# Performance work log

Hardware: AMD Instinct MI355X
Metric: run time of the kernel (lower is better)

## Reference

```python
import jax, jax.numpy as jnp
import numpy as np

B, C, V, L = 32, 32, 1024, 13  # batch, channels, nodes, seq_len
SUPPORT_LEN, ORDER = 3, 2
C_IN_TOTAL = (ORDER * SUPPORT_LEN + 1) * C  # 224
C_OUT = 64


def setup_inputs() -> dict:
    key = jax.random.key(0)
    ks = jax.random.split(key, 6)
    x = jax.random.normal(ks[0], (B, C, V, L), dtype=jnp.float32)
    # row-normalized random adjacencies (dense diffusion matrices)
    def adj(k):
        a = jax.random.uniform(k, (V, V), dtype=jnp.float32)
        return a / jnp.sum(a, axis=1, keepdims=True)
    A0, A1, A2 = adj(ks[1]), adj(ks[2]), adj(ks[3])
    W = jax.random.normal(ks[4], (C_OUT, C_IN_TOTAL), dtype=jnp.float32) * (1.0 / np.sqrt(C_IN_TOTAL))
    b = jnp.zeros((C_OUT,), dtype=jnp.float32)
    return {"x": x, "A0": A0, "A1": A1, "A2": A2, "W": W, "b": b}


def nconv(x, A):
    # x: [b, c, v, l], A: [v, w] -> [b, c, w, l]
    return jnp.einsum('bcvl,vw->bcwl', x, A)


def reference(x, A0, A1, A2, W, b):
    out = [x]
    for A in (A0, A1, A2):
        x1 = nconv(x, A)
        out.append(x1)
        for _ in range(2, ORDER + 1):
            x2 = nconv(x1, A)
            out.append(x2)
            x1 = x2
    h = jnp.concatenate(out, axis=1)  # [b, (order*support_len+1)*c, v, l]
    # 1x1 conv == channel contraction; dropout is identity in eval mode
    return jnp.einsum('bcvl,oc->bovl', h, W) + b[None, :, None, None]
```

## Files before the change

### kernel.cpp

```cpp
#include <hip/hip_runtime.h>
#include <hip/hip_bf16.h>
#include <cstdint>


#define SZE 13631488ull
#define OFF_AT  190840832ull
#define OFF_WB  197132288ull
#define WS_NEED 197160960ull

typedef __attribute__((ext_vector_type(8))) short short8;
typedef __attribute__((ext_vector_type(4))) float f32x4;

__device__ __forceinline__ unsigned short f2b(float f) {
    unsigned int u = __builtin_bit_cast(unsigned int, f);
    u += 0x7FFFu + ((u >> 16) & 1u);
    return (unsigned short)(u >> 16);
}

__device__ __forceinline__ void gl2lds16(const unsigned short* g, unsigned short* l) {
    __builtin_amdgcn_global_load_lds(
        (__attribute__((address_space(1))) void*)(g),
        (__attribute__((address_space(3))) void*)(l), 16, 0, 0);
}

__global__ __launch_bounds__(256) void k_prep(const float* __restrict__ x,
                                              unsigned short* __restrict__ T,
                                              unsigned short* __restrict__ Ht) {
    __shared__ unsigned short sb[32 * 840];
    const int b = blockIdx.x >> 4, vc = blockIdx.x & 15;
    const int t = threadIdx.x;
    const float4* xb = (const float4*)x;
    for (int it = 0; it < 26; ++it) {
        int q = it * 256 + t;
        int c = q / 208, f = q - c * 208;
        float4 u = xb[(size_t)(b * 32 + c) * 3328 + vc * 208 + f];
        ushort4 pk; pk.x = f2b(u.x); pk.y = f2b(u.y); pk.z = f2b(u.z); pk.w = f2b(u.w);
        *(ushort4*)(sb + c * 840 + f * 4) = pk;
    }
    __syncthreads();
    unsigned short* Tb = T + (size_t)b * 13 * 32 * 1024 + (size_t)vc * 64;
    for (int it = 0; it < 26; ++it) {
        int q = it * 256 + t;
        int l = q >> 9, r = q & 511, c = r >> 4, sg = r & 15;
        const unsigned short* src = sb + c * 840 + l;
        ushort4 pk;
        pk.x = src[(sg * 4 + 0) * 13];
        pk.y = src[(sg * 4 + 1) * 13];
        pk.z = src[(sg * 4 + 2) * 13];
        pk.w = src[(sg * 4 + 3) * 13];
        *(ushort4*)(Tb + (size_t)(l * 32 + c) * 1024 + sg * 4) = pk;
    }
    unsigned short* Hb = Ht + ((size_t)b * 13312 + (size_t)vc * 832) * 224;
    for (int it = 0; it < 26; ++it) {
        int q = it * 256 + t;
        int v = q / 104, r = q - v * 104, l = r >> 3, cs = r & 7;
        const unsigned short* src = sb + v * 13 + l;
        ushort4 pk;
        pk.x = src[(cs * 4 + 0) * 840];
        pk.y = src[(cs * 4 + 1) * 840];
        pk.z = src[(cs * 4 + 2) * 840];
        pk.w = src[(cs * 4 + 3) * 840];
        *(ushort4*)(Hb + (size_t)(v * 13 + l) * 224 + cs * 4) = pk;
    }
}

__global__ __launch_bounds__(256) void k_prep_A(const float* __restrict__ A0,
                                                const float* __restrict__ A1,
                                                const float* __restrict__ A2,
                                                unsigned short* __restrict__ AT,
                                                unsigned short* __restrict__ Abf) {
    const float* A = blockIdx.z == 0 ? A0 : blockIdx.z == 1 ? A1 : A2;
    unsigned short* D = AT + (size_t)blockIdx.z * 1024 * 1024;
    unsigned short* D2 = Abf + (size_t)blockIdx.z * 1024 * 1024;
    __shared__ float tile[32][33];
    int v0 = blockIdx.y * 32, w0 = blockIdx.x * 32;
    int c = threadIdx.x & 31, r = threadIdx.x >> 5;
    for (int p = 0; p < 4; ++p) {
        int rr = r + p * 8;
        float val = A[(size_t)(v0 + rr) * 1024 + w0 + c];
        tile[rr][c] = val;
        D2[(size_t)(v0 + rr) * 1024 + w0 + c] = f2b(val);
    }
    __syncthreads();
    for (int p = 0; p < 4; ++p) {
        int rr = r + p * 8;
        D[(size_t)(w0 + rr) * 1024 + v0 + c] = f2b(tile[c][rr]);
    }
}

__global__ __launch_bounds__(256) void k_prep_W(const float* __restrict__ W,
                                                unsigned short* __restrict__ Wb) {
    int idx = blockIdx.x * 256 + threadIdx.x;
    Wb[idx] = f2b(W[idx]);
}

__global__ __launch_bounds__(256) void k_gemm(const unsigned short* __restrict__ Xb, long xz,
                                              const unsigned short* __restrict__ P0,
                                              const unsigned short* __restrict__ P1,
                                              unsigned short* __restrict__ Tout, long tz,
                                              unsigned short* __restrict__ Ht, int doT) {
    __shared__ union {
        struct { unsigned short xs[8192]; unsigned short ps[8192]; } s;
        unsigned short cs[128 * 132];
    } lds;
    const int z = blockIdx.z;
    const unsigned short* X = Xb + (size_t)z * (size_t)xz;
    const unsigned short* P = (z < 3) ? P0 + (size_t)z * 1048576u
                                      : P1 + (size_t)(z - 3) * 1048576u;
    const int i0 = blockIdx.x * 128;
    const int j0 = blockIdx.y * 128;
    const int t = threadIdx.x;
    const int lane = t & 63, wave = t >> 6;
    const int l16 = lane & 15, quad = lane >> 4;
    const int wi = (wave >> 1) * 64, wj = (wave & 1) * 64;

    f32x4 acc[4][4] = {};

    const int row = t >> 2, seg = t & 3;
    const unsigned short* xg0 = X + (size_t)(i0 + row) * 1024 + seg * 8;
    const unsigned short* xg1 = xg0 + (size_t)64 * 1024;
    const unsigned short* pg0 = P + (size_t)(j0 + row) * 1024 + seg * 8;
    const unsigned short* pg1 = pg0 + (size_t)64 * 1024;
    unsigned short* lx0 = lds.s.xs + t * 8;
    unsigned short* lp0 = lds.s.ps + t * 8;

    for (int kt = 0; kt < 16; ++kt) {
        const int ko = kt * 64;
        gl2lds16(xg0 + ko,      lx0);
        gl2lds16(xg1 + ko,      lx0 + 2048);
        gl2lds16(xg0 + ko + 32, lx0 + 4096);
        gl2lds16(xg1 + ko + 32, lx0 + 6144);
        gl2lds16(pg0 + ko,      lp0);
        gl2lds16(pg1 + ko,      lp0 + 2048);
        gl2lds16(pg0 + ko + 32, lp0 + 4096);
        gl2lds16(pg1 + ko + 32, lp0 + 6144);
        __syncthreads();
#pragma unroll
        for (int p = 0; p < 2; ++p) {
            short8 a[4], b[4];
#pragma unroll
            for (int mi = 0; mi < 4; ++mi)
                a[mi] = *(const short8*)(lds.s.xs + p * 4096 + (wi + mi * 16 + l16) * 32 + quad * 8);
#pragma unroll
            for (int nj = 0; nj < 4; ++nj)
                b[nj] = *(const short8*)(lds.s.ps + p * 4096 + (wj + nj * 16 + l16) * 32 + quad * 8);
#pragma unroll
            for (int mi = 0; mi < 4; ++mi)
#pragma unroll
                for (int nj = 0; nj < 4; ++nj)
                    acc[mi][nj] = __builtin_amdgcn_mfma_f32_16x16x32_bf16(a[mi], b[nj], acc[mi][nj], 0, 0, 0);
        }
        __syncthreads();
    }

    if (doT) {
#pragma unroll
        for (int mi = 0; mi < 4; ++mi)
#pragma unroll
            for (int nj = 0; nj < 4; ++nj)
#pragma unroll
                for (int r = 0; r < 4; ++r)
                    lds.cs[(wi + mi * 16 + quad * 4 + r) * 132 + (wj + nj * 16 + l16)] =
                        f2b(acc[mi][nj][r]);
        __syncthreads();
        unsigned short* O = Tout + (size_t)z * (size_t)tz;
#pragma unroll
        for (int rep = 0; rep < 8; ++rep) {
            int q = rep * 256 + t;
            int rr = q >> 4, sg = q & 15;
            *(uint4*)(O + (size_t)(i0 + rr) * 1024 + j0 + sg * 8) =
                *(const uint4*)(lds.cs + rr * 132 + sg * 8);
        }
    }
}

__global__ __launch_bounds__(512, 2) void k_gemm256(
        const unsigned short* __restrict__ Xb,
        const unsigned short* __restrict__ P0,
        const unsigned short* __restrict__ P1,
        unsigned short* __restrict__ Ht) {
    __shared__ unsigned short lds[65536];
    const int comb = blockIdx.x;
    const int z = comb >> 2;
    const int j0 = (comb & 3) * 256;
    const int i0 = blockIdx.y * 256;
    const unsigned short* P = (z < 3) ? P0 + (size_t)z * 1048576u
                                      : P1 + (size_t)(z - 3) * 1048576u;
    const int t = threadIdx.x;
    const int lane = t & 63;
    const int l16 = lane & 15, quad = lane >> 4;
    const int wave = t >> 6, wm = wave >> 2, wn = wave & 3;

    const unsigned short* pa0 = Xb + (size_t)(i0 + (t >> 2)) * 1024 + (t & 3) * 8;
    const unsigned short* pb0 = P  + (size_t)(j0 + (t >> 2)) * 1024 + (t & 3) * 8;

    const int aoff = (wm * 128 + l16) * 32 + quad * 8;
    const int boff = 16384 + (wn * 64 + l16) * 32 + quad * 8;

    auto stage = [&](int H) {
        if (H >= 64) return;
        const int kt = H >> 2, h = H & 3;
        const int ks = h >> 1;
        const unsigned short* s = ((h & 1) ? pb0 : pa0) + kt * 64 + ks * 32;
        unsigned short* d = lds + (kt & 1) * 32768 + (h & 1) * 16384 + ks * 8192 + t * 8;
        gl2lds16(s, d);
        gl2lds16(s + 131072, d + 4096);
    };

    f32x4 acc[8][4] = {};

#pragma unroll
    for (int H = 0; H < 7; ++H) stage(H);
    asm volatile("s_waitcnt vmcnt(6)" ::: "memory");
    __builtin_amdgcn_s_barrier();

#pragma unroll 1
    for (int kt = 0; kt < 16; ++kt) {
        const int base = (kt & 1) * 32768;
        const int P4 = kt * 4;
        short8 a[8], b0, b1;

#pragma unroll
        for (int mi = 0; mi < 8; ++mi)
            a[mi] = *(const short8*)(lds + base + aoff + mi * 512);
        b0 = *(const short8*)(lds + base + boff);
        b1 = *(const short8*)(lds + base + boff + 512);
        stage(P4 + 7);
        __builtin_amdgcn_sched_barrier(0);
        __builtin_amdgcn_s_barrier();
        asm volatile("s_waitcnt lgkmcnt(0)" ::: "memory");
        __builtin_amdgcn_sched_barrier(0);
        __builtin_amdgcn_s_setprio(1);
#pragma unroll
        for (int mi = 0; mi < 8; ++mi) {
            acc[mi][0] = __builtin_amdgcn_mfma_f32_16x16x32_bf16(a[mi], b0, acc[mi][0], 0, 0, 0);
            acc[mi][1] = __builtin_amdgcn_mfma_f32_16x16x32_bf16(a[mi], b1, acc[mi][1], 0, 0, 0);
        }
        __builtin_amdgcn_s_setprio(0);
        __builtin_amdgcn_sched_barrier(0);
        __builtin_amdgcn_s_barrier();

        b0 = *(const short8*)(lds + base + boff + 2 * 512);
        b1 = *(const short8*)(lds + base + boff + 3 * 512);
        stage(P4 + 8);
        __builtin_amdgcn_sched_barrier(0);
        __builtin_amdgcn_s_barrier();
        asm volatile("s_waitcnt lgkmcnt(0)" ::: "memory");
        __builtin_amdgcn_sched_barrier(0);
        __builtin_amdgcn_s_setprio(1);
#pragma unroll
        for (int mi = 0; mi < 8; ++mi) {
            acc[mi][2] = __builtin_amdgcn_mfma_f32_16x16x32_bf16(a[mi], b0, acc[mi][2], 0, 0, 0);
            acc[mi][3] = __builtin_amdgcn_mfma_f32_16x16x32_bf16(a[mi], b1, acc[mi][3], 0, 0, 0);
        }
        __builtin_amdgcn_s_setprio(0);
        __builtin_amdgcn_sched_barrier(0);
        __builtin_amdgcn_s_barrier();

#pragma unroll
        for (int mi = 0; mi < 8; ++mi)
            a[mi] = *(const short8*)(lds + base + 8192 + aoff + mi * 512);
        b0 = *(const short8*)(lds + base + 8192 + boff);
        b1 = *(const short8*)(lds + base + 8192 + boff + 512);
        stage(P4 + 9);
        __builtin_amdgcn_sched_barrier(0);
        __builtin_amdgcn_s_barrier();
        asm volatile("s_waitcnt lgkmcnt(0)" ::: "memory");
        __builtin_amdgcn_sched_barrier(0);
        __builtin_amdgcn_s_setprio(1);
#pragma unroll
        for (int mi = 0; mi < 8; ++mi) {
            acc[mi][0] = __builtin_amdgcn_mfma_f32_16x16x32_bf16(a[mi], b0, acc[mi][0], 0, 0, 0);
            acc[mi][1] = __builtin_amdgcn_mfma_f32_16x16x32_bf16(a[mi], b1, acc[mi][1], 0, 0, 0);
        }
        __builtin_amdgcn_s_setprio(0);
        __builtin_amdgcn_sched_barrier(0);
        __builtin_amdgcn_s_barrier();

        b0 = *(const short8*)(lds + base + 8192 + boff + 2 * 512);
        b1 = *(const short8*)(lds + base + 8192 + boff + 3 * 512);
        stage(P4 + 10);
        if (kt < 14)       asm volatile("s_waitcnt vmcnt(6)" ::: "memory");
        else if (kt == 14) asm volatile("s_waitcnt vmcnt(0)" ::: "memory");
        __builtin_amdgcn_sched_barrier(0);
        __builtin_amdgcn_s_barrier();
        asm volatile("s_waitcnt lgkmcnt(0)" ::: "memory");
        __builtin_amdgcn_sched_barrier(0);
        __builtin_amdgcn_s_setprio(1);
#pragma unroll
        for (int mi = 0; mi < 8; ++mi) {
            acc[mi][2] = __builtin_amdgcn_mfma_f32_16x16x32_bf16(a[mi], b0, acc[mi][2], 0, 0, 0);
            acc[mi][3] = __builtin_amdgcn_mfma_f32_16x16x32_bf16(a[mi], b1, acc[mi][3], 0, 0, 0);
        }
        __builtin_amdgcn_s_setprio(0);
        __builtin_amdgcn_sched_barrier(0);
        __builtin_amdgcn_s_barrier();
    }

    const int cc0 = (z < 3) ? 32 + 64 * z : 64 * (z - 2);
    const int wc = j0 + wn * 64 + l16;
#pragma unroll
    for (int mi = 0; mi < 8; ++mi) {
        int p = (i0 >> 5) + wm * 4 + (mi >> 1);
        int b = p / 13, l = p - b * 13;
        int cc = cc0 + (mi & 1) * 16 + quad * 4;
#pragma unroll
        for (int nj = 0; nj < 4; ++nj) {
            int w = wc + nj * 16;
            size_t m = (size_t)b * 13312 + (size_t)w * 13 + l;
            ushort4 pk;
            pk.x = f2b(acc[mi][nj][0]);
            pk.y = f2b(acc[mi][nj][1]);
            pk.z = f2b(acc[mi][nj][2]);
            pk.w = f2b(acc[mi][nj][3]);
            *(ushort4*)(Ht + m * 224 + cc) = pk;
        }
    }
}

__global__ __launch_bounds__(256) void k_fc(const unsigned short* __restrict__ Ht,
                                            const unsigned short* __restrict__ Wb,
                                            const float* __restrict__ bias,
                                            float* __restrict__ y) {
    __shared__ unsigned short sw[64 * 232];
    const int bid = blockIdx.x;
    const int b = bid >> 5, v0 = (bid & 31) * 32;
    const int t = threadIdx.x;
    const int lane = t & 63, wave = t >> 6;
    const int ms = wave >> 1, os = wave & 1;
    const int l16 = lane & 15, quad = lane >> 4;

    for (int it = 0; it < 7; ++it) {
        int q = it * 256 + t;
        int o = q / 28, sg = q % 28;
        *(uint4*)(sw + o * 232 + sg * 8) = *(const uint4*)(Wb + o * 224 + sg * 8);
    }

    const size_t mw = (size_t)b * 13312 + (size_t)v0 * 13 + ms * 208;
    const unsigned short* ag = Ht + (mw + l16) * 224 + quad * 8;
    float* yb = y + (size_t)b * 851968 + (size_t)v0 * 13 + ms * 208 + quad * 4;

    float bv[2];
#pragma unroll
    for (int nj = 0; nj < 2; ++nj) bv[nj] = bias[os * 32 + nj * 16 + l16];

    short8 c0[7], c1[7];
#pragma unroll
    for (int kk = 0; kk < 7; ++kk) {
        c0[kk] = *(const short8*)(ag + kk * 32);
        c1[kk] = *(const short8*)(ag + 3584 + kk * 32);
    }
    __syncthreads();

    auto body = [&](int mf, short8 (&cur)[7]) {
        short8 nxt[7];
        const bool pf = (mf + 2 < 13);
        if (pf) {
#pragma unroll
            for (int kk = 0; kk < 7; ++kk)
                nxt[kk] = *(const short8*)(ag + (size_t)(mf + 2) * 3584 + kk * 32);
        }
        f32x4 acc[2];
#pragma unroll
        for (int nj = 0; nj < 2; ++nj) acc[nj] = (f32x4){bv[nj], bv[nj], bv[nj], bv[nj]};
#pragma unroll
        for (int kk = 0; kk < 7; ++kk)
#pragma unroll
            for (int nj = 0; nj < 2; ++nj) {
                short8 bf = *(const short8*)(sw + (os * 32 + nj * 16 + l16) * 232 + kk * 32 + quad * 8);
                acc[nj] = __builtin_amdgcn_mfma_f32_16x16x32_bf16(cur[kk], bf, acc[nj], 0, 0, 0);
            }
#pragma unroll
        for (int nj = 0; nj < 2; ++nj)
            *(f32x4*)(yb + (size_t)(os * 32 + nj * 16 + l16) * 13312 + mf * 16) = acc[nj];
        if (pf) {
#pragma unroll
            for (int kk = 0; kk < 7; ++kk) cur[kk] = nxt[kk];
        }
    };
#pragma unroll
    for (int mf = 0; mf < 13; ++mf) {
        if (mf & 1) body(mf, c1); else body(mf, c0);
    }
}

extern "C" void kernel_launch(void* const* d_in, const int* in_sizes, int n_in,
                              void* d_out, int out_size, void* d_ws, size_t ws_size,
                              hipStream_t stream) {
    const float* x    = (const float*)d_in[0];
    const float* A0   = (const float*)d_in[1];
    const float* A1   = (const float*)d_in[2];
    const float* A2   = (const float*)d_in[3];
    const float* W    = (const float*)d_in[4];
    const float* bias = (const float*)d_in[5];

    if (ws_size < WS_NEED) return;

    unsigned short* Ht = (unsigned short*)d_ws;
    unsigned short* AT = (unsigned short*)((char*)d_ws + OFF_AT);
    unsigned short* Wb = (unsigned short*)((char*)d_ws + OFF_WB);
    unsigned short* Tarena = (unsigned short*)d_out;
    unsigned short* Abf = Tarena + SZE;
    unsigned short* AT2 = Tarena + 2 * SZE;

    k_prep<<<512, 256, 0, stream>>>(x, Tarena, Ht);
    k_prep_A<<<dim3(32, 32, 3), 256, 0, stream>>>(A0, A1, A2, AT, Abf);
    k_prep_W<<<56, 256, 0, stream>>>(W, Wb);
    k_gemm<<<dim3(8, 8, 3), 256, 0, stream>>>(AT, 1048576L, Abf, Abf,
                                              AT2, 1048576L, nullptr, 1);
    k_gemm256<<<dim3(24, 52, 1), 512, 0, stream>>>(Tarena, AT, AT2, Ht);
    k_fc<<<1024, 256, 0, stream>>>(Ht, Wb, bias, (float*)d_out);
}
```

Before: 464.9 us.

## Load B operand directly from global to registers and halve LDS in k_gemm256

The 256x256 GEMM kernel no longer stages the B (adjacency) tile in LDS. Each wave now loads its B fragments straight from global memory into registers, double-buffered across k-steps, while only the A tile is staged through LDS with an XOR swizzle to avoid bank conflicts. The fine-grained barrier, setprio and sched_barrier choreography is replaced by a simpler two-buffer loop with one __syncthreads per half-iteration. This halves LDS use and cuts LDS traffic, at the cost of uncoalesced-ish direct global loads for B and less explicit control over instruction scheduling.

```diff
diff --git a/kernel.cpp b/kernel.cpp
--- a/kernel.cpp
+++ b/kernel.cpp
@@ -179,7 +179,7 @@
         const unsigned short* __restrict__ P0,
         const unsigned short* __restrict__ P1,
         unsigned short* __restrict__ Ht) {
-    __shared__ unsigned short lds[65536];
+    __shared__ unsigned short lds[32768];
     const int comb = blockIdx.x;
     const int z = comb >> 2;
     const int j0 = (comb & 3) * 256;
@@ -191,110 +191,63 @@
     const int l16 = lane & 15, quad = lane >> 4;
     const int wave = t >> 6, wm = wave >> 2, wn = wave & 3;
 
-    const unsigned short* pa0 = Xb + (size_t)(i0 + (t >> 2)) * 1024 + (t & 3) * 8;
-    const unsigned short* pb0 = P  + (size_t)(j0 + (t >> 2)) * 1024 + (t & 3) * 8;
-
-    const int aoff = (wm * 128 + l16) * 32 + quad * 8;
-    const int boff = 16384 + (wn * 64 + l16) * 32 + quad * 8;
-
-    auto stage = [&](int H) {
-        if (H >= 64) return;
-        const int kt = H >> 2, h = H & 3;
-        const int ks = h >> 1;
-        const unsigned short* s = ((h & 1) ? pb0 : pa0) + kt * 64 + ks * 32;
-        unsigned short* d = lds + (kt & 1) * 32768 + (h & 1) * 16384 + ks * 8192 + t * 8;
-        gl2lds16(s, d);
-        gl2lds16(s + 131072, d + 4096);
+    const unsigned short* pa0 = Xb + (size_t)(i0 + (t >> 3)) * 1024
+                                   + (size_t)(((t & 7) ^ ((t >> 3) & 7)) * 8);
+    auto stage = [&](int kt, int buf) {
+        const unsigned short* s = pa0 + kt * 64;
+        unsigned short* d = lds + buf * 16384 + t * 8;
+#pragma unroll
+        for (int sw = 0; sw < 4; ++sw)
+            gl2lds16(s + sw * 65536, d + sw * 4096);
     };
 
+    const int abase = (wm * 128 + l16) * 64 + ((quad ^ (l16 & 7)) * 8);
+    const unsigned short* pbl = P + (size_t)(j0 + wn * 64 + l16) * 1024 + quad * 8;
+
     f32x4 acc[8][4] = {};
-
-#pragma unroll
-    for (int H = 0; H < 7; ++H) stage(H);
-    asm volatile("s_waitcnt vmcnt(6)" ::: "memory");
-    __builtin_amdgcn_s_barrier();
+    short8 bA[4], bB[4];
+
+    auto ldb = [&](short8* dst, int g) {
+#pragma unroll
+        for (int nj = 0; nj < 4; ++nj)
+            dst[nj] = *(const short8*)(pbl + nj * 16384 + g * 32);
+    };
+    auto ksstep = [&](const unsigned short* ab, int koff, short8* bu) {
+        short8 a[8];
+#pragma unroll
+        for (int mi = 0; mi < 8; ++mi)
+            a[mi] = *(const short8*)(ab + koff + mi * 1024);
+#pragma unroll
+        for (int mi = 0; mi < 8; ++mi)
+#pragma unroll
+            for (int nj = 0; nj < 4; ++nj)
+                acc[mi][nj] = __builtin_amdgcn_mfma_f32_16x16x32_bf16(a[mi], bu[nj], acc[mi][nj], 0, 0, 0);
+    };
+
+    stage(0, 0);
+    ldb(bA, 0);
+    __syncthreads();
+
+    const unsigned short* bufE = lds;
+    const unsigned short* bufO = lds + 16384;
+    const int koff0 = abase, koff1 = abase ^ 32;
 
 #pragma unroll 1
-    for (int kt = 0; kt < 16; ++kt) {
-        const int base = (kt & 1) * 32768;
-        const int P4 = kt * 4;
-        short8 a[8], b0, b1;
-
-#pragma unroll
-        for (int mi = 0; mi < 8; ++mi)
-            a[mi] = *(const short8*)(lds + base + aoff + mi * 512);
-        b0 = *(const short8*)(lds + base + boff);
-        b1 = *(const short8*)(lds + base + boff + 512);
-        stage(P4 + 7);
-        __builtin_amdgcn_sched_barrier(0);
-        __builtin_amdgcn_s_barrier();
-        asm volatile("s_waitcnt lgkmcnt(0)" ::: "memory");
-        __builtin_amdgcn_sched_barrier(0);
-        __builtin_amdgcn_s_setprio(1);
-#pragma unroll
-        for (int mi = 0; mi < 8; ++mi) {
-            acc[mi][0] = __builtin_amdgcn_mfma_f32_16x16x32_bf16(a[mi], b0, acc[mi][0], 0, 0, 0);
-            acc[mi][1] = __builtin_amdgcn_mfma_f32_16x16x32_bf16(a[mi], b1, acc[mi][1], 0, 0, 0);
-        }
-        __builtin_amdgcn_s_setprio(0);
-        __builtin_amdgcn_sched_barrier(0);
-        __builtin_amdgcn_s_barrier();
-
-        b0 = *(const short8*)(lds + base + boff + 2 * 512);
-        b1 = *(const short8*)(lds + base + boff + 3 * 512);
-        stage(P4 + 8);
-        __builtin_amdgcn_sched_barrier(0);
-        __builtin_amdgcn_s_barrier();
-        asm volatile("s_waitcnt lgkmcnt(0)" ::: "memory");
-        __builtin_amdgcn_sched_barrier(0);
-        __builtin_amdgcn_s_setprio(1);
-#pragma unroll
-        for (int mi = 0; mi < 8; ++mi) {
-            acc[mi][2] = __builtin_amdgcn_mfma_f32_16x16x32_bf16(a[mi], b0, acc[mi][2], 0, 0, 0);
-            acc[mi][3] = __builtin_amdgcn_mfma_f32_16x16x32_bf16(a[mi], b1, acc[mi][3], 0, 0, 0);
-        }
-        __builtin_amdgcn_s_setprio(0);
-        __builtin_amdgcn_sched_barrier(0);
-        __builtin_amdgcn_s_barrier();
-
-#pragma unroll
-        for (int mi = 0; mi < 8; ++mi)
-            a[mi] = *(const short8*)(lds + base + 8192 + aoff + mi * 512);
-        b0 = *(const short8*)(lds + base + 8192 + boff);
-        b1 = *(const short8*)(lds + base + 8192 + boff + 512);
-        stage(P4 + 9);
-        __builtin_amdgcn_sched_barrier(0);
-        __builtin_amdgcn_s_barrier();
-        asm volatile("s_waitcnt lgkmcnt(0)" ::: "memory");
-        __builtin_amdgcn_sched_barrier(0);
-        __builtin_amdgcn_s_setprio(1);
-#pragma unroll
-        for (int mi = 0; mi < 8; ++mi) {
-            acc[mi][0] = __builtin_amdgcn_mfma_f32_16x16x32_bf16(a[mi], b0, acc[mi][0], 0, 0, 0);
-            acc[mi][1] = __builtin_amdgcn_mfma_f32_16x16x32_bf16(a[mi], b1, acc[mi][1], 0, 0, 0);
-        }
-        __builtin_amdgcn_s_setprio(0);
-        __builtin_amdgcn_sched_barrier(0);
-        __builtin_amdgcn_s_barrier();
-
-        b0 = *(const short8*)(lds + base + 8192 + boff + 2 * 512);
-        b1 = *(const short8*)(lds + base + 8192 + boff + 3 * 512);
-        stage(P4 + 10);
-        if (kt < 14)       asm volatile("s_waitcnt vmcnt(6)" ::: "memory");
-        else if (kt == 14) asm volatile("s_waitcnt vmcnt(0)" ::: "memory");
-        __builtin_amdgcn_sched_barrier(0);
-        __builtin_amdgcn_s_barrier();
-        asm volatile("s_waitcnt lgkmcnt(0)" ::: "memory");
-        __builtin_amdgcn_sched_barrier(0);
-        __builtin_amdgcn_s_setprio(1);
-#pragma unroll
-        for (int mi = 0; mi < 8; ++mi) {
-            acc[mi][2] = __builtin_amdgcn_mfma_f32_16x16x32_bf16(a[mi], b0, acc[mi][2], 0, 0, 0);
-            acc[mi][3] = __builtin_amdgcn_mfma_f32_16x16x32_bf16(a[mi], b1, acc[mi][3], 0, 0, 0);
-        }
-        __builtin_amdgcn_s_setprio(0);
-        __builtin_amdgcn_sched_barrier(0);
-        __builtin_amdgcn_s_barrier();
+    for (int kt2 = 0; kt2 < 8; ++kt2) {
+        const int ktE = kt2 * 2;
+        const int g0 = kt2 * 4;
+        stage(ktE + 1, 1);
+        ldb(bB, g0 + 1);
+        ksstep(bufE, koff0, bA);
+        ldb(bA, g0 + 2);
+        ksstep(bufE, koff1, bB);
+        __syncthreads();
+        if (kt2 < 7) stage(ktE + 2, 0);
+        ldb(bB, g0 + 3);
+        ksstep(bufO, koff0, bA);
+        ldb(bA, (g0 + 4) & 31);
+        ksstep(bufO, koff1, bB);
+        __syncthreads();
     }
 
     const int cc0 = (z < 3) ? 32 + 64 * z : 64 * (z - 2);
```

Result: slower. 517.2 us (+11.3%).
